# Kernel tuning notes

Hardware: AMD Instinct MI355X
Metric: run time of the kernel (lower is better)

## Reference

```python
import jax, jax.numpy as jnp
import numpy as np

D_MODEL = 768
D_STATE = 16
EXPAND = 2
D_INNER = D_MODEL * EXPAND
K_CONV = 4
RMS_EPS = 1.1920928955078125e-07  # torch.finfo(float32).eps (nn.RMSNorm default eps=None)


def setup_inputs() -> dict:
    key = jax.random.key(0)
    ks = jax.random.split(key, 8)
    x = jax.random.normal(ks[0], (2, 2048, D_MODEL), dtype=jnp.float32)
    # parameters (torch Linear stores [out, in]; we keep that layout and use x @ W.T)
    in_proj_w = jax.random.normal(ks[1], (2 * D_INNER, D_MODEL), jnp.float32) * (1.0 / np.sqrt(D_MODEL))
    conv_w = jax.random.normal(ks[2], (D_INNER, 1, K_CONV), jnp.float32) * (1.0 / np.sqrt(K_CONV))
    conv_b = jax.random.normal(ks[3], (D_INNER,), jnp.float32) * 0.1
    x_proj_w = jax.random.normal(ks[4], (2 * D_STATE, D_INNER), jnp.float32) * (1.0 / np.sqrt(D_INNER))
    dt_proj_w = jax.random.normal(ks[5], (D_INNER, D_INNER), jnp.float32) * (1.0 / np.sqrt(D_INNER))
    dt_proj_b = jax.random.normal(ks[6], (D_INNER,), jnp.float32) * 0.1
    A_log = jnp.log(jnp.broadcast_to(jnp.arange(1, D_STATE + 1, dtype=jnp.float32)[None, :], (D_INNER, D_STATE)))
    D_skip = jnp.ones((D_INNER,), jnp.float32)
    out_proj_w = jax.random.normal(ks[7], (D_MODEL, D_INNER), jnp.float32) * (1.0 / np.sqrt(D_INNER))
    norm_w = jnp.ones((D_MODEL,), jnp.float32)
    return {"x": x, "norm_w": norm_w, "in_proj_w": in_proj_w, "conv_w": conv_w,
            "conv_b": conv_b, "x_proj_w": x_proj_w, "dt_proj_w": dt_proj_w,
            "dt_proj_b": dt_proj_b, "A_log": A_log, "D_skip": D_skip,
            "out_proj_w": out_proj_w}


def reference(x, norm_w, in_proj_w, conv_w, conv_b, x_proj_w, dt_proj_w,
              dt_proj_b, A_log, D_skip, out_proj_w):
    # x: [B, L, d_model]
    residual = x
    xn = x * jax.lax.rsqrt(jnp.mean(x * x, axis=-1, keepdims=True) + RMS_EPS) * norm_w
    xz = xn @ in_proj_w.T                       # [B, L, 2*d_inner]
    d_inner = in_proj_w.shape[0] // 2
    xb, z = xz[..., :d_inner], xz[..., d_inner:]
    # causal depthwise conv: torch pads 3 both sides then truncates to L == left-pad 3
    xc = jax.lax.conv_general_dilated(
        xb.transpose(0, 2, 1), conv_w, window_strides=(1,), padding=[(K_CONV - 1, 0)],
        feature_group_count=d_inner, dimension_numbers=("NCH", "OIH", "NCH"))
    xc = xc + conv_b[None, :, None]
    u = jax.nn.silu(xc.transpose(0, 2, 1))      # [B, L, d_inner]
    bc = u @ x_proj_w.T                          # [B, L, 2*d_state]
    N = A_log.shape[1]
    Bp, Cp = bc[..., :N], bc[..., N:]
    delta = jax.nn.softplus(u @ dt_proj_w.T + dt_proj_b)  # [B, L, d_inner]
    A = -jnp.exp(A_log)                          # [d_inner, N]

    def step(h, ins):
        dl, ut, Bt, Ct = ins                     # [B,D], [B,D], [B,N], [B,N]
        dA = jnp.exp(dl[:, :, None] * A)         # [B, D, N]
        h = dA * h + dl[:, :, None] * Bt[:, None, :] * ut[:, :, None]
        y = jnp.einsum("bdn,bn->bd", h, Ct)
        return h, y

    B_, L, _ = u.shape
    h0 = jnp.zeros((B_, d_inner, N), x.dtype)
    xs = (delta.transpose(1, 0, 2), u.transpose(1, 0, 2),
          Bp.transpose(1, 0, 2), Cp.transpose(1, 0, 2))
    _, ys = jax.lax.scan(step, h0, xs)           # ys: [L, B, d_inner]
    y = ys.transpose(1, 0, 2) + u * D_skip
    out = (y * jax.nn.silu(z)) @ out_proj_w.T
    return out + residual
```

## Files before the change

### kernel.cpp

```cpp
#include <hip/hip_runtime.h>
#include <math.h>

#define DM 768
#define DI 1536
#define NS 16
#define LL 2048
#define MROWS 4096
#define CH 32
#define NC 64

using bf16x8 = __attribute__((ext_vector_type(8))) short;
using f32x4 = __attribute__((ext_vector_type(4))) float;

__device__ __forceinline__ float4 ld4(const float* p) { return *(const float4*)p; }

__device__ __forceinline__ unsigned short f2bf(float f) {
  unsigned int u = __float_as_uint(f);
  u += 0x7fff + ((u >> 16) & 1);
  return (unsigned short)(u >> 16);
}
__device__ __forceinline__ float b2f(unsigned short s) {
  return __uint_as_float(((unsigned int)s) << 16);
}

__device__ __forceinline__ void gload16(const void* g, void* l) {
  __builtin_amdgcn_global_load_lds((const __attribute__((address_space(1))) void*)g,
                                   (__attribute__((address_space(3))) void*)l, 16, 0, 0);
}

#define N4_IN 589824
#define N4_CAT 638976
#define N4_OUT 294912
__global__ __launch_bounds__(256) void cvt_all(const float* __restrict__ ipw,
                                               const float* __restrict__ dtw,
                                               const float* __restrict__ xpw,
                                               const float* __restrict__ opw,
                                               unsigned short* __restrict__ d_in4,
                                               unsigned short* __restrict__ d_cat,
                                               unsigned short* __restrict__ d_out4) {
  int i = blockIdx.x * 256 + threadIdx.x;
  if (i < N4_IN) {
    float4 v = ld4(ipw + (size_t)i * 4);
    ushort4 o = {f2bf(v.x), f2bf(v.y), f2bf(v.z), f2bf(v.w)};
    *(ushort4*)(d_in4 + (size_t)i * 4) = o;
  } else if (i < N4_IN + N4_CAT) {
    int j = i - N4_IN;
    int row = j / 384;
    int col = (j % 384) * 4;
    ushort4 o = {0, 0, 0, 0};
    if (row < 1536) {
      float4 v = ld4(dtw + (size_t)row * DI + col);
      o = {f2bf(v.x), f2bf(v.y), f2bf(v.z), f2bf(v.w)};
    } else if (row < 1568) {
      float4 v = ld4(xpw + (size_t)(row - 1536) * DI + col);
      o = {f2bf(v.x), f2bf(v.y), f2bf(v.z), f2bf(v.w)};
    }
    *(ushort4*)(d_cat + (size_t)j * 4) = o;
  } else if (i < N4_IN + N4_CAT + N4_OUT) {
    int j = i - N4_IN - N4_CAT;
    float4 v = ld4(opw + (size_t)j * 4);
    ushort4 o = {f2bf(v.x), f2bf(v.y), f2bf(v.z), f2bf(v.w)};
    *(ushort4*)(d_out4 + (size_t)j * 4) = o;
  }
}

__global__ __launch_bounds__(256) void rmsnorm_kernel(const float* __restrict__ x,
                                                      const float* __restrict__ w,
                                                      unsigned short* __restrict__ xn) {
  int row = blockIdx.x;
  const float* xr = x + (size_t)row * DM;
  unsigned short* xo = xn + (size_t)row * DM;
  int tid = threadIdx.x;
  float v0 = xr[tid], v1 = xr[tid + 256], v2 = xr[tid + 512];
  float ss = v0 * v0 + v1 * v1 + v2 * v2;
#pragma unroll
  for (int o = 32; o > 0; o >>= 1) ss += __shfl_xor(ss, o, 64);
  __shared__ float red[4];
  if ((tid & 63) == 0) red[tid >> 6] = ss;
  __syncthreads();
  float tot = red[0] + red[1] + red[2] + red[3];
  float sc = rsqrtf(tot * (1.0f / 768.0f) + 1.1920928955078125e-07f);
  xo[tid] = f2bf(v0 * sc * w[tid]);
  xo[tid + 256] = f2bf(v1 * sc * w[tid + 256]);
  xo[tid + 512] = f2bf(v2 * sc * w[tid + 512]);
}

template <int EPI, int BN>
__global__ __launch_bounds__(256) void mfma_gemm(const unsigned short* __restrict__ A,
                                                 const unsigned short* __restrict__ Bw,
                                                 const float* __restrict__ bias,
                                                 const float* __restrict__ resid,
                                                 void* __restrict__ o0v,
                                                 void* __restrict__ o1v, int K) {
  constexpr int NFJ = BN / 32;
  constexpr int NCH = 16 + BN / 8;
  __shared__ unsigned short As[2][128 * 64];
  __shared__ unsigned short Bs[2][BN * 64];
  int tid = threadIdx.x;
  int lane = tid & 63, w = tid >> 6;
  int wr = w >> 1, wc = w & 1;
  int bm = blockIdx.y * 128, bn = blockIdx.x * BN;

  f32x4 acc[4][NFJ];
#pragma unroll
  for (int i = 0; i < 4; i++)
#pragma unroll
    for (int j = 0; j < NFJ; j++) acc[i][j] = (f32x4){0.f, 0.f, 0.f, 0.f};

  const unsigned short* Ab = A + (size_t)bm * K;
  const unsigned short* Bb = Bw + (size_t)bn * K;
  int lrow = lane >> 3;
  int kof = ((lane & 7) ^ lrow) * 8;

  auto stage = [&](int buf, int k0) {
#pragma unroll
    for (int ch = w; ch < NCH; ch += 4) {
      if (ch < 16) {
        int row = ch * 8 + lrow;
        gload16(Ab + (size_t)row * K + k0 + kof, &As[buf][ch * 512]);
      } else {
        int row = (ch - 16) * 8 + lrow;
        gload16(Bb + (size_t)row * K + k0 + kof, &Bs[buf][(ch - 16) * 512]);
      }
    }
  };
  auto compute = [&](int buf) {
#pragma unroll
    for (int kk = 0; kk < 2; kk++) {
      int sa = (((kk * 4) + (lane >> 4)) ^ (lane & 7)) * 8;
      bf16x8 af[4], bfr[NFJ];
#pragma unroll
      for (int i = 0; i < 4; i++) {
        int arow = wr * 64 + i * 16 + (lane & 15);
        af[i] = *(const bf16x8*)&As[buf][arow * 64 + sa];
      }
#pragma unroll
      for (int j = 0; j < NFJ; j++) {
        int brow = wc * (BN / 2) + j * 16 + (lane & 15);
        bfr[j] = *(const bf16x8*)&Bs[buf][brow * 64 + sa];
      }
#pragma unroll
      for (int i = 0; i < 4; i++)
#pragma unroll
        for (int j = 0; j < NFJ; j++)
          acc[i][j] = __builtin_amdgcn_mfma_f32_16x16x32_bf16(af[i], bfr[j], acc[i][j], 0, 0, 0);
    }
  };

  int nk = K >> 6;
  stage(0, 0);
  __syncthreads();
  for (int t = 0; t < nk; t++) {
    if (t + 1 < nk) stage((t + 1) & 1, (t + 1) << 6);
    compute(t & 1);
    __syncthreads();
  }

#pragma unroll
  for (int i = 0; i < 4; i++) {
#pragma unroll
    for (int j = 0; j < NFJ; j++) {
      int row0 = bm + wr * 64 + i * 16 + (lane >> 4) * 4;
      int col = bn + wc * (BN / 2) + j * 16 + (lane & 15);
#pragma unroll
      for (int r = 0; r < 4; r++) {
        float v = acc[i][j][r];
        int row = row0 + r;
        if (EPI == 0) {
          unsigned short* xb = (unsigned short*)o0v;
          unsigned short* z = (unsigned short*)o1v;
          if (col < DI) xb[(size_t)row * DI + col] = f2bf(v);
          else z[(size_t)row * DI + col - DI] = f2bf(v);
        } else if (EPI == 1) {
          float* delta = (float*)o0v;
          float* bc = (float*)o1v;
          if (col < DI) {
            v += bias[col];
            v = (v > 20.0f) ? v : log1pf(expf(v));
            delta[(size_t)row * DI + col] = v;
          } else if (col < DI + 2 * NS) {
            bc[(size_t)row * 32 + col - DI] = v;
          }
        } else {
          float* out = (float*)o0v;
          out[(size_t)row * DM + col] = v + resid[(size_t)row * DM + col];
        }
      }
    }
  }
}

__global__ __launch_bounds__(192) void conv_silu_kernel(const unsigned short* __restrict__ xb,
                                                        const float* __restrict__ cw,
                                                        const float* __restrict__ cb,
                                                        unsigned short* __restrict__ u) {
  int d = (blockIdx.x * 192 + threadIdx.x) << 2;
  int m = blockIdx.y;
  int t = m & (LL - 1);
  float4 w0 = ld4(cw + d * 4);
  float4 w1 = ld4(cw + d * 4 + 4);
  float4 w2 = ld4(cw + d * 4 + 8);
  float4 w3 = ld4(cw + d * 4 + 12);
  float4 acc = {cb[d], cb[d + 1], cb[d + 2], cb[d + 3]};
#pragma unroll
  for (int tap = 0; tap < 4; tap++) {
    int dt_ = 3 - tap;
    if (t >= dt_) {
      ushort4 xv = *(const ushort4*)(xb + (size_t)(m - dt_) * DI + d);
      float wx = (tap == 0) ? w0.x : (tap == 1) ? w0.y : (tap == 2) ? w0.z : w0.w;
      float wy = (tap == 0) ? w1.x : (tap == 1) ? w1.y : (tap == 2) ? w1.z : w1.w;
      float wz = (tap == 0) ? w2.x : (tap == 1) ? w2.y : (tap == 2) ? w2.z : w2.w;
      float ww = (tap == 0) ? w3.x : (tap == 1) ? w3.y : (tap == 2) ? w3.z : w3.w;
      acc.x += b2f(xv.x) * wx;
      acc.y += b2f(xv.y) * wy;
      acc.z += b2f(xv.z) * wz;
      acc.w += b2f(xv.w) * ww;
    }
  }
  ushort4 o = {f2bf(acc.x / (1.0f + __expf(-acc.x))), f2bf(acc.y / (1.0f + __expf(-acc.y))),
               f2bf(acc.z / (1.0f + __expf(-acc.z))), f2bf(acc.w / (1.0f + __expf(-acc.w)))};
  *(ushort4*)(u + (size_t)m * DI + d) = o;
}

__global__ __launch_bounds__(256) void scan_pass1(const float* __restrict__ delta,
                                                  const unsigned short* __restrict__ u,
                                                  const float* __restrict__ bc,
                                                  const float* __restrict__ A_log,
                                                  float* __restrict__ chunkP,
                                                  float* __restrict__ chunkS) {
  int d = blockIdx.x * 256 + threadIdx.x;
  int c = blockIdx.y;
  int b = blockIdx.z;
  float Acoef[NS];
#pragma unroll
  for (int n = 0; n < NS; n++) Acoef[n] = -__expf(A_log[d * NS + n]);
  __shared__ float sB[CH][NS];
  const float* bcb = bc + (size_t)(b * LL + c * CH) * 32;
  for (int i = threadIdx.x; i < CH * NS; i += 256) sB[i >> 4][i & 15] = bcb[(i >> 4) * 32 + (i & 15)];
  __syncthreads();
  float P[NS], S[NS];
#pragma unroll
  for (int n = 0; n < NS; n++) { P[n] = 1.f; S[n] = 0.f; }
  int m0 = b * LL + c * CH;
  for (int tt = 0; tt < CH; tt++) {
    size_t off = (size_t)(m0 + tt) * DI + d;
    float dl = delta[off];
    float ut = b2f(u[off]);
    float dlu = dl * ut;
#pragma unroll
    for (int n = 0; n < NS; n++) {
      float dA = __expf(dl * Acoef[n]);
      S[n] = dA * S[n] + dlu * sB[tt][n];
      P[n] *= dA;
    }
  }
  size_t base = ((size_t)(b * NC + c) * NS) * DI + d;
#pragma unroll
  for (int n = 0; n < NS; n++) {
    chunkP[base + (size_t)n * DI] = P[n];
    chunkS[base + (size_t)n * DI] = S[n];
  }
}

__global__ __launch_bounds__(256) void scan_pass2(const float* __restrict__ chunkP,
                                                  float* __restrict__ chunkS) {
  int id = blockIdx.x * 256 + threadIdx.x;
  int d = id % DI;
  int n = (id / DI) % NS;
  int b = id / (DI * NS);
  float h = 0.f;
  for (int c = 0; c < NC; c++) {
    size_t idx = ((size_t)(b * NC + c) * NS + n) * DI + d;
    float p = chunkP[idx];
    float s = chunkS[idx];
    chunkS[idx] = h;
    h = p * h + s;
  }
}

__global__ __launch_bounds__(256) void scan_pass3(const float* __restrict__ delta,
                                                  const unsigned short* __restrict__ u,
                                                  const float* __restrict__ bc,
                                                  const float* __restrict__ hIn,
                                                  const float* __restrict__ A_log,
                                                  const float* __restrict__ D_skip,
                                                  const unsigned short* __restrict__ z,
                                                  unsigned short* __restrict__ yg) {
  int d = blockIdx.x * 256 + threadIdx.x;
  int c = blockIdx.y;
  int b = blockIdx.z;
  float Acoef[NS];
#pragma unroll
  for (int n = 0; n < NS; n++) Acoef[n] = -__expf(A_log[d * NS + n]);
  float Dsk = D_skip[d];
  __shared__ float sBC[CH][32];
  const float* bcb = bc + (size_t)(b * LL + c * CH) * 32;
  for (int i = threadIdx.x; i < CH * 32; i += 256) sBC[i >> 5][i & 31] = bcb[i];
  __syncthreads();
  float h[NS];
  size_t base = ((size_t)(b * NC + c) * NS) * DI + d;
#pragma unroll
  for (int n = 0; n < NS; n++) h[n] = hIn[base + (size_t)n * DI];
  int m0 = b * LL + c * CH;
  for (int tt = 0; tt < CH; tt++) {
    size_t m = (size_t)(m0 + tt);
    size_t off = m * DI + d;
    float dl = delta[off];
    float ut = b2f(u[off]);
    float dlu = dl * ut;
    float yt = 0.f;
#pragma unroll
    for (int n = 0; n < NS; n++) {
      float dA = __expf(dl * Acoef[n]);
      h[n] = dA * h[n] + dlu * sBC[tt][n];
      yt += h[n] * sBC[tt][16 + n];
    }
    float zv = b2f(z[m * DI + d]);
    float sz = zv / (1.0f + __expf(-zv));
    yg[m * DI + d] = f2bf((yt + ut * Dsk) * sz);
  }
}

extern "C" void kernel_launch(void* const* d_in, const int* in_sizes, int n_in,
                              void* d_out, int out_size, void* d_ws, size_t ws_size,
                              hipStream_t stream) {
  const float* x = (const float*)d_in[0];
  const float* norm_w = (const float*)d_in[1];
  const float* in_proj_w = (const float*)d_in[2];
  const float* conv_w = (const float*)d_in[3];
  const float* conv_b = (const float*)d_in[4];
  const float* x_proj_w = (const float*)d_in[5];
  const float* dt_proj_w = (const float*)d_in[6];
  const float* dt_proj_b = (const float*)d_in[7];
  const float* A_log = (const float*)d_in[8];
  const float* D_skip = (const float*)d_in[9];
  const float* out_proj_w = (const float*)d_in[10];
  float* out = (float*)d_out;

  float* ws = (float*)d_ws;
  unsigned short* xb_bf = (unsigned short*)ws;
  unsigned short* z_bf = (unsigned short*)(ws + 3145728);
  unsigned short* u_bf = (unsigned short*)(ws + 6291456);
  float* delta = ws + 9437184;
  unsigned short* ygbf = (unsigned short*)(ws + 15728640);
  unsigned short* wbf_in = (unsigned short*)(ws + 18874368);
  unsigned short* wbf_cat = (unsigned short*)(ws + 20054016);
  unsigned short* wbf_out = (unsigned short*)(ws + 21331968);
  float* chunkP = ws + 21921792;
  float* chunkS = ws + 25067520;
  unsigned short* xn_bf = (unsigned short*)d_out;
  float* bcb = (float*)d_out + 1572864;

  cvt_all<<<5953, 256, 0, stream>>>(in_proj_w, dt_proj_w, x_proj_w, out_proj_w,
                                    wbf_in, wbf_cat, wbf_out);

  rmsnorm_kernel<<<4096, 256, 0, stream>>>(x, norm_w, xn_bf);

  mfma_gemm<0, 128><<<dim3(24, 32), 256, 0, stream>>>(xn_bf, wbf_in, nullptr, nullptr,
                                                      xb_bf, z_bf, DM);

  conv_silu_kernel<<<dim3(2, 4096), 192, 0, stream>>>(xb_bf, conv_w, conv_b, u_bf);

  mfma_gemm<1, 128><<<dim3(13, 32), 256, 0, stream>>>(u_bf, wbf_cat, dt_proj_b, nullptr,
                                                      delta, bcb, DI);

  scan_pass1<<<dim3(6, NC, 2), 256, 0, stream>>>(delta, u_bf, bcb, A_log, chunkP, chunkS);
  scan_pass2<<<192, 256, 0, stream>>>(chunkP, chunkS);
  scan_pass3<<<dim3(6, NC, 2), 256, 0, stream>>>(delta, u_bf, bcb, chunkS, A_log, D_skip,
                                                 z_bf, ygbf);

  mfma_gemm<2, 64><<<dim3(12, 32), 256, 0, stream>>>(ygbf, wbf_out, nullptr, x, out,
                                                     nullptr, DI);
}
```

Measured before the change: 242.6 us.

## Single-buffer GEMM LDS tiles and add XCD-aware workgroup swizzle

The MFMA GEMM drops its LDS double buffer for a single buffer. Each k-step now syncs, stages the tile, syncs again and computes, which halves shared memory per block so more blocks can be resident. Block indices are also remapped so consecutive workgroups, which are dispatched round-robin across the 8 XCDs, land on contiguous output tiles for better L2 locality. In exchange, global loads no longer overlap with MFMA compute within a block, and there is an extra barrier per iteration.

```diff
diff --git a/kernel.cpp b/kernel.cpp
--- a/kernel.cpp
+++ b/kernel.cpp
@@ -91,15 +91,20 @@
                                                  const float* __restrict__ bias,
                                                  const float* __restrict__ resid,
                                                  void* __restrict__ o0v,
-                                                 void* __restrict__ o1v, int K) {
+                                                 void* __restrict__ o1v, int K, int gx) {
   constexpr int NFJ = BN / 32;
   constexpr int NCH = 16 + BN / 8;
-  __shared__ unsigned short As[2][128 * 64];
-  __shared__ unsigned short Bs[2][BN * 64];
+  __shared__ unsigned short As[128 * 64];
+  __shared__ unsigned short Bs[BN * 64];
   int tid = threadIdx.x;
   int lane = tid & 63, w = tid >> 6;
   int wr = w >> 1, wc = w & 1;
-  int bm = blockIdx.y * 128, bn = blockIdx.x * BN;
+
+  int nwg = gx * gridDim.y;
+  int orig = blockIdx.y * gx + blockIdx.x;
+  int q = nwg >> 3;
+  int swz = (orig & 7) * q + (orig >> 3);
+  int bm = (swz / gx) * 128, bn = (swz % gx) * BN;
 
   f32x4 acc[4][NFJ];
 #pragma unroll
@@ -112,19 +117,19 @@
   int lrow = lane >> 3;
   int kof = ((lane & 7) ^ lrow) * 8;
 
-  auto stage = [&](int buf, int k0) {
+  auto stage = [&](int k0) {
 #pragma unroll
     for (int ch = w; ch < NCH; ch += 4) {
       if (ch < 16) {
         int row = ch * 8 + lrow;
-        gload16(Ab + (size_t)row * K + k0 + kof, &As[buf][ch * 512]);
+        gload16(Ab + (size_t)row * K + k0 + kof, &As[ch * 512]);
       } else {
         int row = (ch - 16) * 8 + lrow;
-        gload16(Bb + (size_t)row * K + k0 + kof, &Bs[buf][(ch - 16) * 512]);
+        gload16(Bb + (size_t)row * K + k0 + kof, &Bs[(ch - 16) * 512]);
       }
     }
   };
-  auto compute = [&](int buf) {
+  auto compute = [&]() {
 #pragma unroll
     for (int kk = 0; kk < 2; kk++) {
       int sa = (((kk * 4) + (lane >> 4)) ^ (lane & 7)) * 8;
@@ -132,12 +137,12 @@
 #pragma unroll
       for (int i = 0; i < 4; i++) {
         int arow = wr * 64 + i * 16 + (lane & 15);
-        af[i] = *(const bf16x8*)&As[buf][arow * 64 + sa];
+        af[i] = *(const bf16x8*)&As[arow * 64 + sa];
       }
 #pragma unroll
       for (int j = 0; j < NFJ; j++) {
         int brow = wc * (BN / 2) + j * 16 + (lane & 15);
-        bfr[j] = *(const bf16x8*)&Bs[buf][brow * 64 + sa];
+        bfr[j] = *(const bf16x8*)&Bs[brow * 64 + sa];
       }
 #pragma unroll
       for (int i = 0; i < 4; i++)
@@ -148,12 +153,11 @@
   };
 
   int nk = K >> 6;
-  stage(0, 0);
-  __syncthreads();
   for (int t = 0; t < nk; t++) {
-    if (t + 1 < nk) stage((t + 1) & 1, (t + 1) << 6);
-    compute(t & 1);
     __syncthreads();
+    stage(t << 6);
+    __syncthreads();
+    compute();
   }
 
 #pragma unroll
@@ -357,12 +361,12 @@
   rmsnorm_kernel<<<4096, 256, 0, stream>>>(x, norm_w, xn_bf);
 
   mfma_gemm<0, 128><<<dim3(24, 32), 256, 0, stream>>>(xn_bf, wbf_in, nullptr, nullptr,
-                                                      xb_bf, z_bf, DM);
+                                                      xb_bf, z_bf, DM, 24);
 
   conv_silu_kernel<<<dim3(2, 4096), 192, 0, stream>>>(xb_bf, conv_w, conv_b, u_bf);
 
   mfma_gemm<1, 128><<<dim3(13, 32), 256, 0, stream>>>(u_bf, wbf_cat, dt_proj_b, nullptr,
-                                                      delta, bcb, DI);
+                                                      delta, bcb, DI, 13);
 
   scan_pass1<<<dim3(6, NC, 2), 256, 0, stream>>>(delta, u_bf, bcb, A_log, chunkP, chunkS);
   scan_pass2<<<192, 256, 0, stream>>>(chunkP, chunkS);
@@ -370,5 +374,5 @@
                                                  z_bf, ygbf);
 
   mfma_gemm<2, 64><<<dim3(12, 32), 256, 0, stream>>>(ygbf, wbf_out, nullptr, x, out,
-                                                     nullptr, DI);
-}
+                                                     nullptr, DI, 12);
+}
```

After: 225.2 us. -7.2%, faster.
